# Performance work log

Hardware: AMD Instinct MI355X
Metric: run time of the kernel (lower is better)

## Reference

```python
import jax, jax.numpy as jnp
import numpy as np

SQRT2 = np.float32(np.sqrt(2.0))


def _depthwise(x, h, axis):
    """Symmetric-pad depthwise 1D conv along `axis` (2=col/height, 3=row/width).
    Emulates dtcwt_slim ColFilter/RowFilter: prep_filt flips the taps, then
    F.conv2d cross-correlates with groups=C (same taps for every channel).
    x: (B,C,H,W), h: (L,) with L odd -> same-size output."""
    C = x.shape[1]
    L = h.shape[0]
    m = L // 2
    hf = jnp.flip(h)  # prep_filt stores h[::-1]
    if axis == 2:
        xp = jnp.pad(x, ((0, 0), (0, 0), (m, m), (0, 0)), mode='symmetric')
        ker = jnp.tile(hf[None, None, :, None], (C, 1, 1, 1))  # (C,1,L,1)
    else:
        xp = jnp.pad(x, ((0, 0), (0, 0), (0, 0), (m, m)), mode='symmetric')
        ker = jnp.tile(hf[None, None, None, :], (C, 1, 1, 1))  # (C,1,1,L)
    return jax.lax.conv_general_dilated(
        xp, ker, window_strides=(1, 1), padding='VALID',
        dimension_numbers=('NCHW', 'OIHW', 'NCHW'), feature_group_count=C)


def colfilter(x, h):
    return _depthwise(x, h, axis=2)


def rowfilter(x, h):
    return _depthwise(x, h, axis=3)


def c2q(w_r, w_i):
    """Complex pair of subbands -> real quad-interleaved image.
    w_r, w_i: (B,C,2,H,W) -> (B,C,2H,2W)."""
    w1r, w1i = w_r[:, :, 0], w_i[:, :, 0]
    w2r, w2i = w_r[:, :, 1], w_i[:, :, 1]
    x1 = w1r + w2r          # y[::2,  ::2]
    x2 = w1i + w2i          # y[::2, 1::2]
    x3 = w1i - w2i          # y[1::2, ::2]
    x4 = w2r - w1r          # y[1::2,1::2]
    B, C, H, W = x1.shape
    top = jnp.stack([x1, x2], axis=-1).reshape(B, C, H, 2 * W)
    bot = jnp.stack([x3, x4], axis=-1).reshape(B, C, H, 2 * W)
    y = jnp.stack([top, bot], axis=-2).reshape(B, C, 2 * H, 2 * W)
    return y / SQRT2


def setup_inputs() -> dict:
    key = jax.random.key(0)
    k1, k2, k3, k4, k5, k6 = jax.random.split(key, 6)
    B, C, H, W = 8, 64, 256, 256
    Yl = jax.random.normal(k1, (B, C, H, W), dtype=jnp.float32)
    Yhr = jax.random.normal(k2, (B, C, 6, H // 2, W // 2), dtype=jnp.float32)
    Yhi = jax.random.normal(k3, (B, C, 6, H // 2, W // 2), dtype=jnp.float32)
    # near_sym_b_bp synthesis filters (fixed, non-trainable buffers): 13/19/13 taps
    g0o = jax.random.normal(k4, (13,), dtype=jnp.float32) * 0.3
    g1o = jax.random.normal(k5, (19,), dtype=jnp.float32) * 0.3
    g2o = jax.random.normal(k6, (13,), dtype=jnp.float32) * 0.3
    return {"Yl": Yl, "Yhr": Yhr, "Yhi": Yhi, "g0o": g0o, "g1o": g1o, "g2o": g2o}


def reference(Yl, Yhr, Yhi, g0o, g1o, g2o):
    # orientation pairs: (15,165)->lh uses bands 0,5; (75,105)->hl bands 2,3;
    # (45,135 bandpass)->hh bands 1,4
    lh = c2q(Yhr[:, :, 0:6:5], Yhi[:, :, 0:6:5])
    hl = c2q(Yhr[:, :, 2:4:1], Yhi[:, :, 2:4:1])
    hh = c2q(Yhr[:, :, 1:5:3], Yhi[:, :, 1:5:3])
    y1 = colfilter(Yl, g0o) + colfilter(lh, g1o)
    y2 = colfilter(hl, g0o)
    y2bp = colfilter(hh, g2o)
    y = rowfilter(y1, g0o) + rowfilter(y2, g1o) + rowfilter(y2bp, g2o)
    return y
```

## Files before the change

### kernel.cpp

```cpp
#include <hip/hip_runtime.h>

#define TH 32
#define TW 64
#define PW 88

__device__ __forceinline__ int symidx(int t, int n) {
    t = (t < 0) ? (-1 - t) : t;
    return (t >= n) ? (2 * n - 1 - t) : t;
}

__device__ __forceinline__ void col13_yl(
    float (&acc)[TH], const float* __restrict__ ylp,
    const float (&taps)[13], int r0, int cc)
{
    #pragma unroll
    for (int pi = 0; pi < TH + 12; ++pi) {
        int rr = symidx(r0 - 6 + pi, 256);
        float v = ylp[rr * 256 + cc];
        #pragma unroll
        for (int j = 0; j < 13; ++j) {
            int ro = pi + j - 12;
            if (ro >= 0 && ro < TH) acc[ro] = fmaf(taps[j], v, acc[ro]);
        }
    }
}

__device__ __forceinline__ void col13_c2q(
    float (&acc)[TH], const float* __restrict__ yhr, const float* __restrict__ yhi,
    int bA, int bB, const float (&taps)[13], int r0, int cc)
{
    const int cp = cc & 1;
    const int j2 = cc >> 1;
    const float IS2 = 0.70710678118654752f;
    #pragma unroll
    for (int pi = 0; pi < TH + 12; ++pi) {
        int rr = symidx(r0 - 6 + pi, 256);
        int rp = rr & 1;
        int i2 = rr >> 1;
        const float* base = (((rp ^ cp) != 0) ? yhi : yhr) + (i2 * 128 + j2);
        float A  = base[bA * 16384];
        float Bv = base[bB * 16384];
        float vA = (rp & cp)       ? -A  : A;
        float vB = (rp & (cp ^ 1)) ? -Bv : Bv;
        float v = (vA + vB) * IS2;
        #pragma unroll
        for (int j = 0; j < 13; ++j) {
            int ro = pi + j - 12;
            if (ro >= 0 && ro < TH) acc[ro] = fmaf(taps[j], v, acc[ro]);
        }
    }
}

__device__ __forceinline__ void col19_c2q(
    float (&acc)[TH], const float* __restrict__ yhr, const float* __restrict__ yhi,
    const float (&taps)[19], int r0, int cc)
{
    const int bA = 0, bB = 5;
    const int cp = cc & 1;
    const int j2 = cc >> 1;
    const float IS2 = 0.70710678118654752f;
    #pragma unroll
    for (int pi = 0; pi < TH + 18; ++pi) {
        int rr = symidx(r0 - 9 + pi, 256);
        int rp = rr & 1;
        int i2 = rr >> 1;
        const float* base = (((rp ^ cp) != 0) ? yhi : yhr) + (i2 * 128 + j2);
        float A  = base[bA * 16384];
        float Bv = base[bB * 16384];
        float vA = (rp & cp)       ? -A  : A;
        float vB = (rp & (cp ^ 1)) ? -Bv : Bv;
        float v = (vA + vB) * IS2;
        #pragma unroll
        for (int j = 0; j < 19; ++j) {
            int ro = pi + j - 18;
            if (ro >= 0 && ro < TH) acc[ro] = fmaf(taps[j], v, acc[ro]);
        }
    }
}

extern "C" __global__ __launch_bounds__(512) void dtcwt_inv(
    const float* __restrict__ Yl, const float* __restrict__ Yhr,
    const float* __restrict__ Yhi,
    const float* __restrict__ g0, const float* __restrict__ g1,
    const float* __restrict__ g2, float* __restrict__ out)
{
    __shared__ __align__(16) float sT[4][TH][PW];

    const int tid = threadIdx.x;
    const int plane = blockIdx.z;
    const int r0 = blockIdx.y * TH;
    const int c0 = blockIdx.x * TW;

    const float* ylp = Yl  + (size_t)plane * 65536;
    const float* yhr = Yhr + (size_t)plane * 6 * 16384;
    const float* yhi = Yhi + (size_t)plane * 6 * 16384;

    float G0[13], G1[19], G2[13];
    #pragma unroll
    for (int j = 0; j < 13; ++j) G0[j] = g0[j];
    #pragma unroll
    for (int j = 0; j < 19; ++j) G1[j] = g1[j];
    #pragma unroll
    for (int j = 0; j < 13; ++j) G2[j] = g2[j];

    const int role = tid >> 7;
    const int lr   = tid & 127;

    float acc[TH];
    #pragma unroll
    for (int i = 0; i < TH; ++i) acc[i] = 0.0f;

    int ti = -1;
    if (role == 0) {
        if (lr < 76) {
            ti = lr + 6;
            int cc = symidx(c0 + ti - 12, 256);
            col13_yl(acc, ylp, G0, r0, cc);
        }
    } else if (role == 1) {
        if (lr < 76) {
            ti = lr + 6;
            int cc = symidx(c0 + ti - 12, 256);
            col19_c2q(acc, yhr, yhi, G1, r0, cc);
        }
    } else if (role == 2) {
        if (lr < 82) {
            ti = lr + 3;
            int cc = symidx(c0 + ti - 12, 256);
            col13_c2q(acc, yhr, yhi, 2, 3, G0, r0, cc);
        }
    } else {
        if (lr < 76) {
            ti = lr + 6;
            int cc = symidx(c0 + ti - 12, 256);
            col13_c2q(acc, yhr, yhi, 1, 4, G2, r0, cc);
        }
    }
    if (ti >= 0) {
        #pragma unroll
        for (int ro = 0; ro < TH; ++ro) sT[role][ro][ti] = acc[ro];
    }
    __syncthreads();

    const int cg = tid & 15;
    const int r  = tid >> 4;
    const int cb = 4 * cg;

    float w1[20];
    #pragma unroll
    for (int k = 0; k < 5; ++k) {
        float4 a = *(const float4*)&sT[0][r][cb + 4 + 4 * k];
        float4 b = *(const float4*)&sT[1][r][cb + 4 + 4 * k];
        w1[4*k+0] = a.x + b.x; w1[4*k+1] = a.y + b.y;
        w1[4*k+2] = a.z + b.z; w1[4*k+3] = a.w + b.w;
    }
    float w2[28];
    #pragma unroll
    for (int k = 0; k < 7; ++k) {
        float4 a = *(const float4*)&sT[2][r][cb + 4 * k];
        w2[4*k+0] = a.x; w2[4*k+1] = a.y; w2[4*k+2] = a.z; w2[4*k+3] = a.w;
    }
    float w3[20];
    #pragma unroll
    for (int k = 0; k < 5; ++k) {
        float4 a = *(const float4*)&sT[3][r][cb + 4 + 4 * k];
        w3[4*k+0] = a.x; w3[4*k+1] = a.y; w3[4*k+2] = a.z; w3[4*k+3] = a.w;
    }

    float4 res;
    float* rp = (float*)&res;
    #pragma unroll
    for (int q = 0; q < 4; ++q) {
        float s = 0.0f;
        #pragma unroll
        for (int j = 0; j < 13; ++j) s = fmaf(G0[j], w1[q + 14 - j], s);
        #pragma unroll
        for (int j = 0; j < 19; ++j) s = fmaf(G1[j], w2[q + 21 - j], s);
        #pragma unroll
        for (int j = 0; j < 13; ++j) s = fmaf(G2[j], w3[q + 14 - j], s);
        rp[q] = s;
    }
    *(float4*)&out[(size_t)plane * 65536 + (size_t)(r0 + r) * 256 + (c0 + cb)] = res;
}

extern "C" void kernel_launch(void* const* d_in, const int* in_sizes, int n_in,
                              void* d_out, int out_size, void* d_ws, size_t ws_size,
                              hipStream_t stream) {
    const float* Yl  = (const float*)d_in[0];
    const float* Yhr = (const float*)d_in[1];
    const float* Yhi = (const float*)d_in[2];
    const float* g0  = (const float*)d_in[3];
    const float* g1  = (const float*)d_in[4];
    const float* g2  = (const float*)d_in[5];
    float* out = (float*)d_out;

    dim3 grid(256 / TW, 256 / TH, 8 * 64);
    dim3 block(512, 1, 1);
    dtcwt_inv<<<grid, block, 0, stream>>>(Yl, Yhr, Yhi, g0, g1, g2, out);
}
```

Before: 351.2 us.

## Stage column-pass inputs through LDS with software-pipelined loads and all-thread compute

Rewrites the column-filter stage. All 512 threads now cooperatively load the Yl tile and each pair of highpass subbands into a shared buffer, then split the column convolution across threads in 8-row slices, instead of a quarter of the threads each streaming a full 32-row column from global memory. The next subband's global loads are issued into registers before the current subband is computed, so memory latency is hidden behind the FMAs. The change also adds an XCD-aware block-index swizzle over a flat 1D grid, separate fast and border paths chosen by template, and sets a minimum occupancy in launch bounds. The cost is a larger LDS footprint and extra barriers, and register pressure may rise because the filter taps are now read directly from global pointers.

```diff
diff --git a/kernel.cpp b/kernel.cpp
--- a/kernel.cpp
+++ b/kernel.cpp
@@ -1,146 +1,197 @@
 #include <hip/hip_runtime.h>
 
-#define TH 32
-#define TW 64
 #define PW 88
+#define IS2 0.70710678118654752f
+
+__device__ __forceinline__ int imin(int a, int b) { return a < b ? a : b; }
+__device__ __forceinline__ int imax(int a, int b) { return a > b ? a : b; }
 
 __device__ __forceinline__ int symidx(int t, int n) {
     t = (t < 0) ? (-1 - t) : t;
     return (t >= n) ? (2 * n - 1 - t) : t;
 }
 
-__device__ __forceinline__ void col13_yl(
-    float (&acc)[TH], const float* __restrict__ ylp,
-    const float (&taps)[13], int r0, int cc)
-{
-    #pragma unroll
-    for (int pi = 0; pi < TH + 12; ++pi) {
-        int rr = symidx(r0 - 6 + pi, 256);
-        float v = ylp[rr * 256 + cc];
-        #pragma unroll
-        for (int j = 0; j < 13; ++j) {
-            int ro = pi + j - 12;
-            if (ro >= 0 && ro < TH) acc[ro] = fmaf(taps[j], v, acc[ro]);
-        }
-    }
-}
-
-__device__ __forceinline__ void col13_c2q(
-    float (&acc)[TH], const float* __restrict__ yhr, const float* __restrict__ yhi,
-    int bA, int bB, const float (&taps)[13], int r0, int cc)
-{
-    const int cp = cc & 1;
-    const int j2 = cc >> 1;
-    const float IS2 = 0.70710678118654752f;
-    #pragma unroll
-    for (int pi = 0; pi < TH + 12; ++pi) {
-        int rr = symidx(r0 - 6 + pi, 256);
-        int rp = rr & 1;
-        int i2 = rr >> 1;
-        const float* base = (((rp ^ cp) != 0) ? yhi : yhr) + (i2 * 128 + j2);
-        float A  = base[bA * 16384];
-        float Bv = base[bB * 16384];
-        float vA = (rp & cp)       ? -A  : A;
-        float vB = (rp & (cp ^ 1)) ? -Bv : Bv;
-        float v = (vA + vB) * IS2;
-        #pragma unroll
-        for (int j = 0; j < 13; ++j) {
-            int ro = pi + j - 12;
-            if (ro >= 0 && ro < TH) acc[ro] = fmaf(taps[j], v, acc[ro]);
-        }
-    }
-}
-
-__device__ __forceinline__ void col19_c2q(
-    float (&acc)[TH], const float* __restrict__ yhr, const float* __restrict__ yhi,
-    const float (&taps)[19], int r0, int cc)
-{
-    const int bA = 0, bB = 5;
-    const int cp = cc & 1;
-    const int j2 = cc >> 1;
-    const float IS2 = 0.70710678118654752f;
-    #pragma unroll
-    for (int pi = 0; pi < TH + 18; ++pi) {
-        int rr = symidx(r0 - 9 + pi, 256);
-        int rp = rr & 1;
-        int i2 = rr >> 1;
-        const float* base = (((rp ^ cp) != 0) ? yhi : yhr) + (i2 * 128 + j2);
-        float A  = base[bA * 16384];
-        float Bv = base[bB * 16384];
-        float vA = (rp & cp)       ? -A  : A;
-        float vB = (rp & (cp ^ 1)) ? -Bv : Bv;
-        float v = (vA + vB) * IS2;
-        #pragma unroll
-        for (int j = 0; j < 19; ++j) {
-            int ro = pi + j - 18;
-            if (ro >= 0 && ro < TH) acc[ro] = fmaf(taps[j], v, acc[ro]);
-        }
-    }
-}
-
-extern "C" __global__ __launch_bounds__(512) void dtcwt_inv(
+__device__ __forceinline__ void wg_barrier() {
+    asm volatile("s_waitcnt lgkmcnt(0)" ::: "memory");
+    __builtin_amdgcn_s_barrier();
+    asm volatile("" ::: "memory");
+}
+
+__device__ __forceinline__ void issue_sub(float (&rc)[13], const float* __restrict__ bp,
+                                          int i2lo, int i2hi, int jc, int rowpar)
+{
+    #pragma unroll
+    for (int r = 0; r < 13; ++r) {
+        int i2c = imin(i2lo + rowpar + 2 * r, i2hi);
+        rc[r] = bp[i2c * 128 + jc];
+    }
+}
+
+__device__ __forceinline__ void write_sub(float* sC, const float (&rc)[13],
+                                          int sej, int which, int rowpar, bool sAct)
+{
+    if (sAct) {
+        #pragma unroll
+        for (int r = 0; r < 13; ++r) {
+            sC[(rowpar + 2 * r) * 176 + sej * 4 + which] = rc[r];
+        }
+    }
+}
+
+template<int L, int RO, bool BORDER>
+__device__ __forceinline__ void compute_c2q(
+    float* sTk, const float* sC, const float* __restrict__ taps,
+    int sI, int jj, int ej, int cp, bool act, int r0, int i2lo)
+{
+    if (!act) return;
+    constexpr int W = 8 + L - 1;
+    float acc[8];
+    #pragma unroll
+    for (int k = 0; k < 8; ++k) acc[k] = 0.f;
+    const float mO = cp ? -IS2 : IS2;
+    const int laneE = ej * 4 + cp * 2;
+    const int laneO = laneE ^ 2;
+    const int rowbase = sI * 704;
+    #pragma unroll
+    for (int t = 0; t < W; ++t) {
+        float v;
+        if (BORDER) {
+            int rr = symidx(r0 - RO + 8 * sI + t, 256);
+            int rp = rr & 1;
+            int ei = (rr >> 1) - i2lo;
+            float2 AB = *reinterpret_cast<const float2*>(&sC[ei * 176 + (rp ? laneO : laneE)]);
+            v = rp ? (AB.x - AB.y) * mO : (AB.x + AB.y) * IS2;
+        } else {
+            const int rp  = (RO + t) & 1;
+            const int eiC = ((t - RO) >> 1) + 5;
+            float2 AB = *reinterpret_cast<const float2*>(
+                &sC[rowbase + eiC * 176 + (rp ? laneO : laneE)]);
+            v = rp ? (AB.x - AB.y) * mO : (AB.x + AB.y) * IS2;
+        }
+        #pragma unroll
+        for (int k = 0; k < 8; ++k) {
+            const int j = k + L - 1 - t;
+            if (j >= 0 && j < L) acc[k] = fmaf(taps[j], v, acc[k]);
+        }
+    }
+    #pragma unroll
+    for (int k = 0; k < 8; ++k) sTk[(8 * sI + k) * PW + (jj + 3)] = acc[k];
+}
+
+__device__ __forceinline__ void compute_yl(
+    float* sT0, const float* sY, const float* __restrict__ g0,
+    int sI, int jj, bool act)
+{
+    if (!act) return;
+    float acc[8];
+    #pragma unroll
+    for (int k = 0; k < 8; ++k) acc[k] = 0.f;
+    const int base = sI * 672 + jj;
+    #pragma unroll
+    for (int t = 0; t < 20; ++t) {
+        float v = sY[base + t * 84];
+        #pragma unroll
+        for (int k = 0; k < 8; ++k) {
+            const int j = k + 12 - t;
+            if (j >= 0 && j < 13) acc[k] = fmaf(g0[j], v, acc[k]);
+        }
+    }
+    #pragma unroll
+    for (int k = 0; k < 8; ++k) sT0[(8 * sI + k) * PW + (jj + 3)] = acc[k];
+}
+
+extern "C" __global__ __launch_bounds__(512, 4) void dtcwt_inv(
     const float* __restrict__ Yl, const float* __restrict__ Yhr,
     const float* __restrict__ Yhi,
     const float* __restrict__ g0, const float* __restrict__ g1,
     const float* __restrict__ g2, float* __restrict__ out)
 {
-    __shared__ __align__(16) float sT[4][TH][PW];
+    __shared__ __align__(16) float sT[4][32][PW];
+    __shared__ __align__(16) float uB[4576];
 
     const int tid = threadIdx.x;
-    const int plane = blockIdx.z;
-    const int r0 = blockIdx.y * TH;
-    const int c0 = blockIdx.x * TW;
+    const int wg  = blockIdx.x;
+    const int swz = (wg & 7) * 2048 + (wg >> 3);
+    const int plane = swz >> 5;
+    const int bt = swz & 31;
+    const int bx = bt & 3;
+    const int by = bt >> 2;
+    const int r0 = by * 32;
+    const int c0 = bx * 64;
 
     const float* ylp = Yl  + (size_t)plane * 65536;
     const float* yhr = Yhr + (size_t)plane * 6 * 16384;
     const float* yhi = Yhi + (size_t)plane * 6 * 16384;
 
-    float G0[13], G1[19], G2[13];
-    #pragma unroll
-    for (int j = 0; j < 13; ++j) G0[j] = g0[j];
-    #pragma unroll
-    for (int j = 0; j < 19; ++j) G1[j] = g1[j];
-    #pragma unroll
-    for (int j = 0; j < 13; ++j) G2[j] = g2[j];
-
-    const int role = tid >> 7;
-    const int lr   = tid & 127;
-
-    float acc[TH];
-    #pragma unroll
-    for (int i = 0; i < TH; ++i) acc[i] = 0.0f;
-
-    int ti = -1;
-    if (role == 0) {
-        if (lr < 76) {
-            ti = lr + 6;
-            int cc = symidx(c0 + ti - 12, 256);
-            col13_yl(acc, ylp, G0, r0, cc);
-        }
-    } else if (role == 1) {
-        if (lr < 76) {
-            ti = lr + 6;
-            int cc = symidx(c0 + ti - 12, 256);
-            col19_c2q(acc, yhr, yhi, G1, r0, cc);
-        }
-    } else if (role == 2) {
-        if (lr < 82) {
-            ti = lr + 3;
-            int cc = symidx(c0 + ti - 12, 256);
-            col13_c2q(acc, yhr, yhi, 2, 3, G0, r0, cc);
-        }
-    } else {
-        if (lr < 76) {
-            ti = lr + 6;
-            int cc = symidx(c0 + ti - 12, 256);
-            col13_c2q(acc, yhr, yhi, 1, 4, G2, r0, cc);
-        }
-    }
-    if (ti >= 0) {
-        #pragma unroll
-        for (int ro = 0; ro < TH; ++ro) sT[role][ro][ti] = acc[ro];
-    }
-    __syncthreads();
+    const int rloF = imax(0, r0 - 9), rhiF = imin(255, r0 + 40);
+    const int i2lo = rloF >> 1, i2hi = rhiF >> 1;
+    const int clo  = imax(0, c0 - 9), chi = imin(255, c0 + 72);
+    const int j2lo = clo >> 1, j2hi = chi >> 1;
+
+    const int jj = tid & 127;
+    const int sI = tid >> 7;
+    const bool act = jj < 82;
+    const int ccq = symidx(c0 - 9 + jj, 256);
+    const int cp  = ccq & 1;
+    const int ej  = (ccq >> 1) - j2lo;
+
+    const int sej = tid & 63;
+    const int which = (tid >> 6) & 3;
+    const int rowpar = (tid >> 8) & 1;
+    const int jc = imin(j2lo + sej, j2hi);
+    const bool sAct = sej < 42;
+
+    const bool border = (by == 0) || (by == 7);
+
+    const float* bpLh = ((which & 2) ? yhi : yhr) + ((which & 1) ? 5 : 0) * 16384;
+    const float* bpHl = ((which & 2) ? yhi : yhr) + ((which & 1) ? 3 : 2) * 16384;
+    const float* bpHh = ((which & 2) ? yhi : yhr) + ((which & 1) ? 4 : 1) * 16384;
+
+    float rYl[11], rA[13], rB[13];
+
+    #pragma unroll
+    for (int r = 0; r < 11; ++r) {
+        int rrY = symidx(r0 - 6 + sI + 4 * r, 256);
+        rYl[r] = ylp[rrY * 256 + ccq];
+    }
+    issue_sub(rA, bpLh, i2lo, i2hi, jc, rowpar);
+    __builtin_amdgcn_sched_barrier(0);
+
+    if (act) {
+        #pragma unroll
+        for (int r = 0; r < 11; ++r) uB[(sI + 4 * r) * 84 + jj] = rYl[r];
+    }
+    wg_barrier();
+
+    issue_sub(rB, bpHl, i2lo, i2hi, jc, rowpar);
+    __builtin_amdgcn_sched_barrier(0);
+
+    compute_yl(&sT[0][0][0], uB, g0, sI, jj, act);
+    wg_barrier();
+
+    write_sub(uB, rA, sej, which, rowpar, sAct);
+    wg_barrier();
+
+    issue_sub(rA, bpHh, i2lo, i2hi, jc, rowpar);
+    __builtin_amdgcn_sched_barrier(0);
+
+    if (border) compute_c2q<19, 9, true >(&sT[1][0][0], uB, g1, sI, jj, ej, cp, act, r0, i2lo);
+    else        compute_c2q<19, 9, false>(&sT[1][0][0], uB, g1, sI, jj, ej, cp, act, r0, i2lo);
+    wg_barrier();
+
+    write_sub(uB, rB, sej, which, rowpar, sAct);
+    wg_barrier();
+
+    if (border) compute_c2q<13, 6, true >(&sT[2][0][0], uB, g0, sI, jj, ej, cp, act, r0, i2lo);
+    else        compute_c2q<13, 6, false>(&sT[2][0][0], uB, g0, sI, jj, ej, cp, act, r0, i2lo);
+    wg_barrier();
+
+    write_sub(uB, rA, sej, which, rowpar, sAct);
+    wg_barrier();
+
+    if (border) compute_c2q<13, 6, true >(&sT[3][0][0], uB, g2, sI, jj, ej, cp, act, r0, i2lo);
+    else        compute_c2q<13, 6, false>(&sT[3][0][0], uB, g2, sI, jj, ej, cp, act, r0, i2lo);
+    wg_barrier();
 
     const int cg = tid & 15;
     const int r  = tid >> 4;
@@ -171,14 +222,14 @@
     float* rp = (float*)&res;
     #pragma unroll
     for (int q = 0; q < 4; ++q) {
-        float s = 0.0f;
-        #pragma unroll
-        for (int j = 0; j < 13; ++j) s = fmaf(G0[j], w1[q + 14 - j], s);
-        #pragma unroll
-        for (int j = 0; j < 19; ++j) s = fmaf(G1[j], w2[q + 21 - j], s);
-        #pragma unroll
-        for (int j = 0; j < 13; ++j) s = fmaf(G2[j], w3[q + 14 - j], s);
-        rp[q] = s;
+        float sacc = 0.0f;
+        #pragma unroll
+        for (int j = 0; j < 13; ++j) sacc = fmaf(g0[j], w1[q + 14 - j], sacc);
+        #pragma unroll
+        for (int j = 0; j < 19; ++j) sacc = fmaf(g1[j], w2[q + 21 - j], sacc);
+        #pragma unroll
+        for (int j = 0; j < 13; ++j) sacc = fmaf(g2[j], w3[q + 14 - j], sacc);
+        rp[q] = sacc;
     }
     *(float4*)&out[(size_t)plane * 65536 + (size_t)(r0 + r) * 256 + (c0 + cb)] = res;
 }
@@ -194,7 +245,7 @@
     const float* g2  = (const float*)d_in[5];
     float* out = (float*)d_out;
 
-    dim3 grid(256 / TW, 256 / TH, 8 * 64);
+    dim3 grid(16384, 1, 1);
     dim3 block(512, 1, 1);
     dtcwt_inv<<<grid, block, 0, stream>>>(Yl, Yhr, Yhi, g0, g1, g2, out);
 }
```

Result: slower. 430.6 us (+22.6%).
